# Kernel optimization log

Measured on AMD Instinct MI355X. Metric: run time of the kernel, lower is better.

## Reference

```python
import jax, jax.numpy as jnp
import numpy as np

B, C, H, W = 8, 512, 64, 64
K = 8
NUM = K * K          # number of channel groups / graph nodes
CG = C // NUM        # channels per group (8)
NC = 19              # num_classes
OUT = 512            # bottleneck out_channels


def make_dct_weight():
    # Per-channel 2D DCT basis. Channel ch belongs to group g = ch // CG;
    # group g selects frequency (u, v) = (g % K, g // K).
    g = np.arange(C) // CG
    u = (g % K).astype(np.float64)
    v = (g // K).astype(np.float64)
    th = (np.arange(H) + 0.5) / H   # [H]
    tw = (np.arange(W) + 0.5) / W   # [W]
    bh = np.cos(np.pi * u[:, None] * th[None, :])  # [C,H]
    bw = np.cos(np.pi * v[:, None] * tw[None, :])  # [C,W]
    return (bh[:, :, None] * bw[:, None, :]).astype(np.float32)  # [C,H,W]


def setup_inputs() -> dict:
    key = jax.random.key(0)
    ks = jax.random.split(key, 10)
    s = lambda i, shape: jax.random.normal(ks[i], shape, jnp.float32) * 0.05
    return {
        'x': jax.random.normal(ks[0], (B, C, H, W), jnp.float32),
        'dct_w': jnp.asarray(make_dct_weight()),
        'dm_w1': s(1, (CG, CG)),
        'dm_gamma': jnp.ones((CG,), jnp.float32),
        'dm_beta': jnp.zeros((CG,), jnp.float32),
        'dm_w2': s(2, (NC, CG)),
        'dm_b2': s(3, (NC,)),
        'fuse_w': s(4, (NUM,)),
        'fuse_b': s(5, (1,)),
        'gcn_w1': s(6, (NUM, NUM)),
        'gcn_w2': s(7, (CG, CG)),
        'bot_w': s(8, (OUT, 2 * C, 3, 3)),
        'bot_gamma': jnp.ones((OUT,), jnp.float32),
        'bot_beta': jnp.zeros((OUT,), jnp.float32),
    }


def reference(x, dct_w, dm_w1, dm_gamma, dm_beta, dm_w2, dm_b2,
              fuse_w, fuse_b, gcn_w1, gcn_w2, bot_w, bot_gamma, bot_beta):
    # MultiSpectralDCTLayer: elementwise DCT basis multiply, keeps [B,C,H,W]
    fres = x * dct_w[None]

    # channel_split -> grouped layout [B, NUM, CG, H*W]
    xg = x.reshape(B, NUM, CG, H * W)
    fg = fres.reshape(B, NUM, CG, H * W)

    # decoder_map: 1x1 conv -> BN(eval, mean=0,var=1) -> ReLU -> (Dropout=id) -> 1x1 conv
    h1 = jnp.einsum('dc,bncp->bndp', dm_w1, fg)
    h1 = jax.nn.relu(h1 * dm_gamma[None, None, :, None] + dm_beta[None, None, :, None])
    fres_map = jnp.einsum('kc,bncp->bnkp', dm_w2, h1) + dm_b2[None, None, :, None]  # [B,n,NC,HW]

    # fuse: 1x1 conv over group dim n -> [B,NC,H,W]
    fres_map_output = (jnp.einsum('n,bnkp->bkp', fuse_w, fres_map) + fuse_b[0]).reshape(B, NC, H, W)

    # local frequency class centers: [B,n,NC,HW] @ [B,n,HW,c] -> [B,n,NC,c]
    fHWc = fg.transpose(0, 1, 3, 2)   # [B,n,HW,c]
    xHWc = xg.transpose(0, 1, 3, 2)   # [B,n,HW,c]
    local = jnp.einsum('bnkp,bnpc->bnkc', fres_map, fHWc)

    # GCN over n (node) dim: conv1 + residual ReLU, then Linear over c
    g = jnp.einsum('mn,bnkc->bmkc', gcn_w1, local)
    g = jax.nn.relu(g + local)
    local = jnp.einsum('bnkc,dc->bnkd', g, gcn_w2)

    # attention combine: softmax(x @ local^T) @ local
    wm = jax.nn.softmax(jnp.einsum('bnpc,bnkc->bnpk', xHWc, local), axis=-1)  # [B,n,HW,NC]
    out = jnp.einsum('bnpk,bnkc->bnpc', wm, local)  # [B,n,HW,c]

    # channel_recover -> [B,C,H,W]
    out = out.transpose(0, 1, 3, 2).reshape(B, C, H, W)

    # bottleneck: 3x3 conv on concat, BN(eval) affine, ReLU
    cat = jnp.concatenate([x, out], axis=1)  # [B,2C,H,W]
    y = jax.lax.conv_general_dilated(cat, bot_w, (1, 1), 'SAME',
                                     dimension_numbers=('NCHW', 'OIHW', 'NCHW'))
    y = jax.nn.relu(y * bot_gamma[None, :, None, None] + bot_beta[None, :, None, None])
    return (y, fres_map_output)
```

## Files before the change

kernel.cpp:

```cpp
#include <hip/hip_runtime.h>


typedef __attribute__((ext_vector_type(8))) unsigned short u16x8;
typedef __attribute__((ext_vector_type(8))) __bf16 bf16x8;
typedef __attribute__((ext_vector_type(4))) float f32x4;

__device__ inline unsigned short f2bf(float f) {
    unsigned int u = __float_as_uint(f);
    u += 0x7fffu + ((u >> 16) & 1u);
    return (unsigned short)(u >> 16);
}

__device__ __forceinline__ void gload16(unsigned short* lds, const unsigned short* g) {
    __builtin_amdgcn_global_load_lds(
        (const __attribute__((address_space(1))) unsigned int*)g,
        (__attribute__((address_space(3))) unsigned int*)lds, 16, 0, 0);
}

__global__ __launch_bounds__(256) void repack_w(const float* __restrict__ w,
                                                unsigned short* __restrict__ wt) {
    __shared__ float buf[9216];
    const int oc = blockIdx.x;
    const int tid = threadIdx.x;
    const float* src = w + (size_t)oc * 9216;
    for (int i = tid; i < 9216; i += 256) buf[i] = src[i];
    __syncthreads();
#pragma unroll
    for (int t = 0; t < 9; ++t) {
        for (int i = tid; i < 1024; i += 256)
            wt[((size_t)t * 512 + oc) * 1024 + i] = f2bf(buf[i * 9 + t]);
    }
}

__global__ __launch_bounds__(256) void front_kernel(
    const float* __restrict__ x, const float* __restrict__ dct,
    const float* __restrict__ w1, const float* __restrict__ gamma,
    const float* __restrict__ beta, const float* __restrict__ w2,
    const float* __restrict__ b2, const float* __restrict__ fuse_w,
    float* __restrict__ part, float* __restrict__ fpart,
    unsigned short* __restrict__ cat) {
    __shared__ __align__(16) float fgs[8][260];
    __shared__ __align__(16) float fms[19][260];
    __shared__ float sw1[64], sw2[152], sb2[19], sg[8], sb[8], sfw[64];
    const int bid = blockIdx.x;
    const int sp = bid >> 7;
    const int b = (bid >> 4) & 7;
    const int ch = bid & 15;
    const int tid = threadIdx.x;
    if (tid < 64) { sw1[tid] = w1[tid]; sfw[tid] = fuse_w[tid]; }
    if (tid < 152) sw2[tid] = w2[tid];
    if (tid < 19) sb2[tid] = b2[tid];
    if (tid < 8) { sg[tid] = gamma[tid]; sb[tid] = beta[tid]; }
    __syncthreads();
    const int p = ch * 256 + tid;
    const int kk = tid >> 3, cc = tid & 7;
    float facc[19];
#pragma unroll
    for (int k = 0; k < 19; ++k) facc[k] = 0.f;
    for (int nn = 0; nn < 16; ++nn) {
        const int n = sp * 16 + nn;
        float fg[8];
        u16x8 xw;
#pragma unroll
        for (int c = 0; c < 8; ++c) {
            const float xv = x[((size_t)(b * 512 + n * 8 + c)) * 4096 + p];
            fg[c] = xv * dct[((size_t)(n * 8 + c)) * 4096 + p];
            xw[c] = f2bf(xv);
            fgs[c][tid] = fg[c];
        }
        *(u16x8*)(cat + ((size_t)(b * 4096) + p) * 1024 + n * 8) = xw;
        float h1[8];
#pragma unroll
        for (int d = 0; d < 8; ++d) {
            float s = 0.f;
#pragma unroll
            for (int c = 0; c < 8; ++c) s = fmaf(sw1[d * 8 + c], fg[c], s);
            h1[d] = fmaxf(fmaf(s, sg[d], sb[d]), 0.f);
        }
        const float fw = sfw[n];
#pragma unroll
        for (int k = 0; k < 19; ++k) {
            float s = sb2[k];
#pragma unroll
            for (int d = 0; d < 8; ++d) s = fmaf(sw2[k * 8 + d], h1[d], s);
            fms[k][tid] = s;
            facc[k] = fmaf(fw, s, facc[k]);
        }
        __syncthreads();
        if (tid < 152) {
            float accv = 0.f;
#pragma unroll 8
            for (int p4 = 0; p4 < 256; p4 += 4) {
                const float4 a = *(const float4*)&fms[kk][p4];
                const float4 g4 = *(const float4*)&fgs[cc][p4];
                accv += a.x * g4.x + a.y * g4.y + a.z * g4.z + a.w * g4.w;
            }
            part[((size_t)((b * 64 + n) * 16) + ch) * 152 + tid] = accv;
        }
        __syncthreads();
    }
#pragma unroll
    for (int k = 0; k < 19; ++k)
        fpart[((size_t)(sp * 8 + b) * 19 + k) * 4096 + p] = facc[k];
}

__global__ __launch_bounds__(256) void fuse_reduce(
    const float* __restrict__ fpart, const float* __restrict__ fuse_b,
    float* __restrict__ out1) {
    const int i = blockIdx.x * 256 + threadIdx.x;
    float s = fuse_b[0];
#pragma unroll
    for (int sp = 0; sp < 4; ++sp) s += fpart[(size_t)sp * 622592 + i];
    out1[i] = s;
}

__global__ __launch_bounds__(256) void lsum_kernel(
    const float* __restrict__ part, float* __restrict__ L) {
    const int i = blockIdx.x * 256 + threadIdx.x;
    const int bn = i / 152;
    const int t = i - bn * 152;
    float s = 0.f;
#pragma unroll
    for (int ch = 0; ch < 16; ++ch)
        s += part[((size_t)(bn * 16 + ch)) * 152 + t];
    L[i] = s;
}

__global__ __launch_bounds__(256) void gcn2_kernel(
    const float* __restrict__ Lg, const float* __restrict__ w1,
    const float* __restrict__ w2, float* __restrict__ local2) {
    __shared__ float L[9728];
    __shared__ float R[1216];
    __shared__ float sw1[4096];
    __shared__ float sw2[64];
    const int b = blockIdx.x >> 3;
    const int n0 = (blockIdx.x & 7) * 8;
    const int tid = threadIdx.x;
    for (int i = tid; i < 9728; i += 256) L[i] = Lg[(size_t)b * 9728 + i];
    for (int i = tid; i < 4096; i += 256) sw1[i] = w1[i];
    if (tid < 64) sw2[tid] = w2[tid];
    __syncthreads();
    for (int i = tid; i < 1216; i += 256) {
        const int nn = i / 152, t = i - nn * 152;
        const int m = n0 + nn;
        float g = 0.f;
        for (int n = 0; n < 64; ++n) g = fmaf(sw1[m * 64 + n], L[n * 152 + t], g);
        R[i] = fmaxf(g + L[m * 152 + t], 0.f);
    }
    __syncthreads();
    for (int i = tid; i < 1216; i += 256) {
        const int nn = i / 152, t = i - nn * 152;
        const int k = t >> 3, d = t & 7;
        float s = 0.f;
#pragma unroll
        for (int c = 0; c < 8; ++c) s = fmaf(R[nn * 152 + k * 8 + c], sw2[d * 8 + c], s);
        local2[(size_t)b * 9728 + (n0 + nn) * 152 + t] = s;
    }
}

__global__ __launch_bounds__(256) void attn_kernel(
    const float* __restrict__ x, const float* __restrict__ local2,
    unsigned short* __restrict__ cat) {
    __shared__ float L[152];
    const int bn = blockIdx.x;
    const int b = bn >> 6, n = bn & 63;
    const int tid = threadIdx.x;
    if (tid < 152) L[tid] = local2[(size_t)bn * 152 + tid];
    __syncthreads();
    for (int i = 0; i < 16; ++i) {
        const int p = i * 256 + tid;
        float xv[8];
#pragma unroll
        for (int c = 0; c < 8; ++c)
            xv[c] = x[((size_t)(b * 512 + n * 8 + c)) * 4096 + p];
        float lg[19];
        float mx = -1e30f;
#pragma unroll
        for (int k = 0; k < 19; ++k) {
            float s = 0.f;
#pragma unroll
            for (int c = 0; c < 8; ++c) s = fmaf(xv[c], L[k * 8 + c], s);
            lg[k] = s;
            mx = fmaxf(mx, s);
        }
        float se = 0.f;
#pragma unroll
        for (int k = 0; k < 19; ++k) {
            lg[k] = __expf(lg[k] - mx);
            se += lg[k];
        }
        const float inv = 1.f / se;
        float ov[8];
#pragma unroll
        for (int c = 0; c < 8; ++c) ov[c] = 0.f;
#pragma unroll
        for (int k = 0; k < 19; ++k) {
#pragma unroll
            for (int c = 0; c < 8; ++c) ov[c] = fmaf(lg[k], L[k * 8 + c], ov[c]);
        }
        u16x8 w;
#pragma unroll
        for (int c = 0; c < 8; ++c) w[c] = f2bf(ov[c] * inv);
        *(u16x8*)(cat + ((size_t)(b * 4096) + p) * 1024 + 512 + n * 8) = w;
    }
}

__global__ __launch_bounds__(512, 1) void conv_kernel(
    const unsigned short* __restrict__ cat, const unsigned short* __restrict__ wt,
    const unsigned short* __restrict__ zp,
    const float* __restrict__ gamma, const float* __restrict__ beta,
    float* __restrict__ out) {
    __shared__ __align__(16) unsigned short As[10 * 4096];
    __shared__ __align__(16) unsigned short Bs[2 * 16384];
    const int bid0 = blockIdx.x;
    const int bid = (bid0 & 7) * 32 + (bid0 >> 3);
    const int mt = bid >> 1;
    const int nt = bid & 1;
    const int b = mt >> 4;
    const int pix0 = (mt & 15) * 256;
    const int y0 = (mt & 15) * 4;
    const int ocb = nt * 256;
    const int tid = threadIdx.x;
    const int w = tid >> 6;
    const int lane = tid & 63;
    const int l16 = lane & 15;
    const int khalf = lane >> 4;
    const int wr1 = w >> 2;
    const int wrow = wr1 * 64;
    const int wcol = (w & 3) * 32;
    const int sx = tid >> 3;
    const int icsw = ((tid & 7) ^ ((tid >> 3) & 7)) * 8;
    const unsigned short* zps = zp + icsw;
    const unsigned short* catb = cat + ((size_t)b * 4096) * 1024 + icsw;
    int colk[3][2];
#pragma unroll
    for (int d = 0; d < 3; ++d)
#pragma unroll
        for (int ks = 0; ks < 2; ++ks)
            colk[d][ks] = ((ks * 64 + khalf * 16) ^ (((l16 + d - 1) & 7) << 4)) >> 1;

    f32x4 acc[2][2][4][2];
#pragma unroll
    for (int qm = 0; qm < 2; ++qm)
#pragma unroll
        for (int qn = 0; qn < 2; ++qn)
#pragma unroll
            for (int m = 0; m < 4; ++m)
#pragma unroll
                for (int n = 0; n < 2; ++n)
#pragma unroll
                    for (int j = 0; j < 4; ++j) acc[qm][qn][m][n][j] = 0.f;

    bf16x8 af0[4][2];
    bf16x8 af1[4][2];
    bf16x8 bq[2][2];
    const bf16x8 zf = {};

#define AF_READ(AFD, QM, DY, DX)                                                   \
    {                                                                              \
        const int r_ = (QM) * 2 + wr1 + (DY) + 1;                                  \
        const int phys_ = (r_ < 2) ? r_ : r_ + 4 * cp;                             \
        const int rb_ = phys_ * 4096;                                              \
        _Pragma("unroll") for (int m_ = 0; m_ < 4; ++m_) {                         \
            const int xm_ = m_ * 16 + l16 + (DX);                                  \
            const int xc_ = ((DX) == 0) ? xm_ : min(max(xm_, 0), 63);              \
            const int ab_ = rb_ + xc_ * 64;                                        \
            _Pragma("unroll") for (int ks_ = 0; ks_ < 2; ++ks_)                    \
                AFD[m_][ks_] = *(const bf16x8*)(As + ab_ + colk[(DX) + 1][ks_]);   \
            if ((DX) == -1 && m_ == 0 && l16 == 0) { AFD[0][0] = zf; AFD[0][1] = zf; } \
            if ((DX) == 1 && m_ == 3 && l16 == 15) { AFD[3][0] = zf; AFD[3][1] = zf; } \
        }                                                                          \
    }

#define BQ_READ(SOFF, QN)                                                          \
    _Pragma("unroll") for (int n_ = 0; n_ < 2; ++n_)                               \
        _Pragma("unroll") for (int ks_ = 0; ks_ < 2; ++ks_)                        \
            bq[n_][ks_] = *(const bf16x8*)(Bs + (SOFF) +                           \
                ((QN) * 128 + wcol + n_ * 16 + l16) * 64 + colk[1][ks_]);

#define STAGE_BH(H, SWOFF, TAP, ICB)                                               \
    _Pragma("unroll") for (int j_ = 0; j_ < 2; ++j_) {                             \
        gload16(Bs + (SWOFF) + (H) * 8192 + (j_ * 512 + tid) * 8,                  \
                wt + (size_t)(TAP) * 524288 +                                      \
                    (size_t)(ocb + (H) * 128 + j_ * 64 + sx) * 1024 + (ICB) + icsw); \
    }

#define STAGE_AROW(R)                                                              \
    do {                                                                           \
        const int yy_ = y0 - 1 + (R);                                              \
        const int ph_ = ((R) < 2) ? (R) : (R) + 4 * cp1;                           \
        const unsigned short* s2_ = ((unsigned)yy_ < 64u)                          \
            ? catb + ((size_t)(yy_ * 64 + sx)) * 1024 + iccn : zps;                \
        gload16(As + ph_ * 4096 + tid * 8, s2_);                                   \
    } while (0)

#define MFMA_Q(AFD, QM, QN)                                                        \
    __builtin_amdgcn_s_setprio(1);                                                 \
    _Pragma("unroll") for (int m_ = 0; m_ < 4; ++m_)                               \
        _Pragma("unroll") for (int n_ = 0; n_ < 2; ++n_)                           \
            _Pragma("unroll") for (int ks_ = 0; ks_ < 2; ++ks_)                    \
                acc[QM][QN][m_][n_] = __builtin_amdgcn_mfma_f32_16x16x32_bf16(     \
                    AFD[m_][ks_], bq[n_][ks_], acc[QM][QN][m_][n_], 0, 0, 0);      \
    __builtin_amdgcn_s_setprio(0);

#define VWAIT(N)                                                                   \
    asm volatile("s_waitcnt vmcnt(" #N ")" ::: "memory");                          \
    __builtin_amdgcn_sched_barrier(0);

#define TAP_BODY(T, DY, DX, AROW, W0N, W2N)                                        \
    {                                                                              \
        const int s_ = (c + (T)) & 1;                                              \
        const int sr_ = s_ << 14;                                                  \
        const int sw_ = sr_ ^ 16384;                                               \
        const int tn_ = ((T) == 8) ? 0 : (T) + 1;                                  \
        const int icb_ = ((T) == 8) ? iccn : icc;                                  \
                                                                  \
        VWAIT(W0N)                                                                 \
        __builtin_amdgcn_s_barrier();                                              \
        __builtin_amdgcn_sched_barrier(0);                                         \
        AF_READ(af0, 0, DY, DX)                                                    \
        BQ_READ(sr_, 0)                                                            \
        STAGE_BH(0, sw_, tn_, icb_)                                                \
        MFMA_Q(af0, 0, 0)                                                          \
                                                                  \
        AF_READ(af1, 1, DY, DX)                                                    \
        if ((AROW) >= 0) STAGE_AROW(AROW);                                         \
        MFMA_Q(af1, 1, 0)                                                          \
                                                                  \
        VWAIT(W2N)                                                                 \
        BQ_READ(sr_, 1)                                                            \
        STAGE_BH(1, sw_, tn_, icb_)                                                \
        MFMA_Q(af1, 1, 1)                                                          \
                                             \
        MFMA_Q(af0, 0, 1)                                                          \
    }

    {
        const int cp1 = 0, iccn = 0;
#pragma unroll
        for (int r = 0; r < 6; ++r) STAGE_AROW(r);
    }
    STAGE_BH(0, 0, 0, 0)
    STAGE_BH(1, 0, 0, 0)

    for (int c = 0; c < 16; ++c) {
        const int cp = c & 1;
        const int cp1 = cp ^ 1;
        const int icc = c << 6;
        const int iccn = ((c + 1) & 15) << 6;
        TAP_BODY(0, -1, -1, -1, 2, 2)
        TAP_BODY(1, -1, 0, -1, 2, 2)
        TAP_BODY(2, -1, 1, -1, 2, 2)
        TAP_BODY(3, 0, -1, 0, 2, 3)
        TAP_BODY(4, 0, 0, 2, 3, 3)
        TAP_BODY(5, 0, 1, 3, 3, 3)
        TAP_BODY(6, 1, -1, 1, 3, 3)
        TAP_BODY(7, 1, 0, 4, 3, 3)
        TAP_BODY(8, 1, 1, 5, 3, 3)
    }
    asm volatile("s_waitcnt vmcnt(0)" ::: "memory");

#pragma unroll
    for (int qn = 0; qn < 2; ++qn)
#pragma unroll
        for (int n = 0; n < 2; ++n) {
            const int oc = ocb + qn * 128 + wcol + n * 16 + l16;
            const float g = gamma[oc], bb = beta[oc];
#pragma unroll
            for (int qm = 0; qm < 2; ++qm)
#pragma unroll
                for (int m = 0; m < 4; ++m) {
                    const int P = qm * 128 + wrow + m * 16 + khalf * 4;
                    float4 o;
                    o.x = fmaxf(fmaf(acc[qm][qn][m][n][0], g, bb), 0.f);
                    o.y = fmaxf(fmaf(acc[qm][qn][m][n][1], g, bb), 0.f);
                    o.z = fmaxf(fmaf(acc[qm][qn][m][n][2], g, bb), 0.f);
                    o.w = fmaxf(fmaf(acc[qm][qn][m][n][3], g, bb), 0.f);
                    *(float4*)(out + ((size_t)(b * 512 + oc)) * 4096 + pix0 + P) = o;
                }
        }
#undef AF_READ
#undef BQ_READ
#undef STAGE_BH
#undef STAGE_AROW
#undef MFMA_Q
#undef VWAIT
#undef TAP_BODY
}

extern "C" void kernel_launch(void* const* d_in, const int* in_sizes, int n_in,
                              void* d_out, int out_size, void* d_ws, size_t ws_size,
                              hipStream_t stream) {
    const float* x = (const float*)d_in[0];
    const float* dct = (const float*)d_in[1];
    const float* dm_w1 = (const float*)d_in[2];
    const float* dm_g = (const float*)d_in[3];
    const float* dm_b = (const float*)d_in[4];
    const float* dm_w2 = (const float*)d_in[5];
    const float* dm_b2 = (const float*)d_in[6];
    const float* fuse_w = (const float*)d_in[7];
    const float* fuse_b = (const float*)d_in[8];
    const float* gcn_w1 = (const float*)d_in[9];
    const float* gcn_w2 = (const float*)d_in[10];
    const float* bot_w = (const float*)d_in[11];
    const float* bot_g = (const float*)d_in[12];
    const float* bot_b = (const float*)d_in[13];

    float* y = (float*)d_out;
    float* out1 = y + (size_t)8 * 512 * 4096;
    float* part = y;
    float* fpart = y + 1245184;
    float* Lbuf = y + 3735552;

    char* ws = (char*)d_ws;
    const size_t CAT_BYTES = (size_t)8 * 4096 * 1024 * 2;
    const size_t WT_BYTES = (size_t)9 * 512 * 1024 * 2;
    const size_t PART_BYTES = (size_t)2048 * 152 * 4;
    const size_t L2_BYTES = (size_t)8 * 9728 * 4;
    const size_t ZP_BYTES = 4096;
    if (ws_size < CAT_BYTES + WT_BYTES + PART_BYTES + L2_BYTES + ZP_BYTES) return;

    unsigned short* cat = (unsigned short*)ws;
    unsigned short* wt = (unsigned short*)(ws + CAT_BYTES);
    float* local2 = (float*)(ws + CAT_BYTES + WT_BYTES + PART_BYTES);
    unsigned short* zp = (unsigned short*)(ws + CAT_BYTES + WT_BYTES + PART_BYTES + L2_BYTES);

    hipMemsetAsync(zp, 0, ZP_BYTES, stream);
    front_kernel<<<dim3(512), dim3(256), 0, stream>>>(x, dct, dm_w1, dm_g, dm_b,
                                                      dm_w2, dm_b2, fuse_w,
                                                      part, fpart, cat);
    lsum_kernel<<<dim3(304), dim3(256), 0, stream>>>(part, Lbuf);
    gcn2_kernel<<<dim3(64), dim3(256), 0, stream>>>(Lbuf, gcn_w1, gcn_w2, local2);
    fuse_reduce<<<dim3(2432), dim3(256), 0, stream>>>(fpart, fuse_b, out1);
    repack_w<<<dim3(512), dim3(256), 0, stream>>>(bot_w, wt);
    attn_kernel<<<dim3(512), dim3(256), 0, stream>>>(x, local2, cat);
    conv_kernel<<<dim3(256), dim3(512), 0, stream>>>(cat, wt, zp, bot_g, bot_b, y);
}
```

Before: 396.1 us.

## Read bf16 x from cat in attention and reuse one A-fragment buffer in conv

The attention kernel now reads x as packed bf16 from the already-written cat buffer with one 16-byte vector load instead of eight strided fp32 loads. This changes the attention input from fp32 to bf16-rounded values. The conv kernel drops its second A-fragment register array and re-reads the quadrant-0 fragment from LDS before the last MFMA group. This cuts register pressure at the cost of extra LDS reads.

Measured after the change: 394.1 us (median of 2 runs). Within noise of the previous version (-0.5%).

```diff
diff --git a/kernel.cpp b/kernel.cpp
--- a/kernel.cpp
+++ b/kernel.cpp
@@ -9,6 +9,10 @@
     unsigned int u = __float_as_uint(f);
     u += 0x7fffu + ((u >> 16) & 1u);
     return (unsigned short)(u >> 16);
+}
+
+__device__ inline float bf2f(unsigned short u) {
+    return __uint_as_float(((unsigned int)u) << 16);
 }
 
 __device__ __forceinline__ void gload16(unsigned short* lds, const unsigned short* g) {
@@ -159,8 +163,7 @@
 }
 
 __global__ __launch_bounds__(256) void attn_kernel(
-    const float* __restrict__ x, const float* __restrict__ local2,
-    unsigned short* __restrict__ cat) {
+    const float* __restrict__ local2, unsigned short* __restrict__ cat) {
     __shared__ float L[152];
     const int bn = blockIdx.x;
     const int b = bn >> 6, n = bn & 63;
@@ -169,10 +172,10 @@
     __syncthreads();
     for (int i = 0; i < 16; ++i) {
         const int p = i * 256 + tid;
+        const u16x8 xr = *(const u16x8*)(cat + ((size_t)(b * 4096) + p) * 1024 + n * 8);
         float xv[8];
 #pragma unroll
-        for (int c = 0; c < 8; ++c)
-            xv[c] = x[((size_t)(b * 512 + n * 8 + c)) * 4096 + p];
+        for (int c = 0; c < 8; ++c) xv[c] = bf2f(xr[c]);
         float lg[19];
         float mx = -1e30f;
 #pragma unroll
@@ -251,12 +254,11 @@
 #pragma unroll
                     for (int j = 0; j < 4; ++j) acc[qm][qn][m][n][j] = 0.f;
 
-    bf16x8 af0[4][2];
-    bf16x8 af1[4][2];
+    bf16x8 af[4][2];
     bf16x8 bq[2][2];
     const bf16x8 zf = {};
 
-#define AF_READ(AFD, QM, DY, DX)                                                   \
+#define AF_READ(QM, DY, DX)                                                        \
     {                                                                              \
         const int r_ = (QM) * 2 + wr1 + (DY) + 1;                                  \
         const int phys_ = (r_ < 2) ? r_ : r_ + 4 * cp;                             \
@@ -266,9 +268,9 @@
             const int xc_ = ((DX) == 0) ? xm_ : min(max(xm_, 0), 63);              \
             const int ab_ = rb_ + xc_ * 64;                                        \
             _Pragma("unroll") for (int ks_ = 0; ks_ < 2; ++ks_)                    \
-                AFD[m_][ks_] = *(const bf16x8*)(As + ab_ + colk[(DX) + 1][ks_]);   \
-            if ((DX) == -1 && m_ == 0 && l16 == 0) { AFD[0][0] = zf; AFD[0][1] = zf; } \
-            if ((DX) == 1 && m_ == 3 && l16 == 15) { AFD[3][0] = zf; AFD[3][1] = zf; } \
+                af[m_][ks_] = *(const bf16x8*)(As + ab_ + colk[(DX) + 1][ks_]);    \
+            if ((DX) == -1 && m_ == 0 && l16 == 0) { af[0][0] = zf; af[0][1] = zf; } \
+            if ((DX) == 1 && m_ == 3 && l16 == 15) { af[3][0] = zf; af[3][1] = zf; } \
         }                                                                          \
     }
 
@@ -294,13 +296,13 @@
         gload16(As + ph_ * 4096 + tid * 8, s2_);                                   \
     } while (0)
 
-#define MFMA_Q(AFD, QM, QN)                                                        \
+#define MFMA_Q(QM, QN)                                                             \
     __builtin_amdgcn_s_setprio(1);                                                 \
     _Pragma("unroll") for (int m_ = 0; m_ < 4; ++m_)                               \
         _Pragma("unroll") for (int n_ = 0; n_ < 2; ++n_)                           \
             _Pragma("unroll") for (int ks_ = 0; ks_ < 2; ++ks_)                    \
                 acc[QM][QN][m_][n_] = __builtin_amdgcn_mfma_f32_16x16x32_bf16(     \
-                    AFD[m_][ks_], bq[n_][ks_], acc[QM][QN][m_][n_], 0, 0, 0);      \
+                    af[m_][ks_], bq[n_][ks_], acc[QM][QN][m_][n_], 0, 0, 0);       \
     __builtin_amdgcn_s_setprio(0);
 
 #define VWAIT(N)                                                                   \
@@ -318,21 +320,22 @@
         VWAIT(W0N)                                                                 \
         __builtin_amdgcn_s_barrier();                                              \
         __builtin_amdgcn_sched_barrier(0);                                         \
-        AF_READ(af0, 0, DY, DX)                                                    \
+        AF_READ(0, DY, DX)                                                         \
         BQ_READ(sr_, 0)                                                            \
         STAGE_BH(0, sw_, tn_, icb_)                                                \
-        MFMA_Q(af0, 0, 0)                                                          \
+        MFMA_Q(0, 0)                                                               \
                                                                   \
-        AF_READ(af1, 1, DY, DX)                                                    \
+        AF_READ(1, DY, DX)                                                         \
         if ((AROW) >= 0) STAGE_AROW(AROW);                                         \
-        MFMA_Q(af1, 1, 0)                                                          \
+        MFMA_Q(1, 0)                                                               \
                                                                   \
         VWAIT(W2N)                                                                 \
         BQ_READ(sr_, 1)                                                            \
         STAGE_BH(1, sw_, tn_, icb_)                                                \
-        MFMA_Q(af1, 1, 1)                                                          \
-                                             \
-        MFMA_Q(af0, 0, 1)                                                          \
+        MFMA_Q(1, 1)                                                               \
+                                                                  \
+        AF_READ(0, DY, DX)                                                         \
+        MFMA_Q(0, 1)                                                               \
     }
 
     {
@@ -433,6 +436,6 @@
     gcn2_kernel<<<dim3(64), dim3(256), 0, stream>>>(Lbuf, gcn_w1, gcn_w2, local2);
     fuse_reduce<<<dim3(2432), dim3(256), 0, stream>>>(fpart, fuse_b, out1);
     repack_w<<<dim3(512), dim3(256), 0, stream>>>(bot_w, wt);
-    attn_kernel<<<dim3(512), dim3(256), 0, stream>>>(x, local2, cat);
+    attn_kernel<<<dim3(512), dim3(256), 0, stream>>>(local2, cat);
     conv_kernel<<<dim3(256), dim3(512), 0, stream>>>(cat, wt, zp, bot_g, bot_b, y);
 }
```
